# Kernel tuning notes

Measured on AMD Instinct MI355X. Metric: run time of the kernel, lower is better.

The kernel has to match this reference:

```python
import jax, jax.numpy as jnp
import numpy as np
from jax import lax

T_HORIZON = 5.0
OFFSET_X = 1.0  # longitudinal safety offset in VEH_VEH_distance
OFFSET_Y = 0.3  # lateral safety offset


def _rollout(state, dt, n_steps):
    """Unicycle Euler rollout with zero backup control (const vel, const yaw).
    state: [B, A, 4] = (x, y, yaw, v); dt: [B, A, 1]. Returns [B, A, T, 4]."""
    def step_fn(s, _):
        yaw = s[..., 2]
        v = s[..., 3]
        zeros = jnp.zeros_like(v)
        ds = jnp.stack([v * jnp.cos(yaw), v * jnp.sin(yaw), zeros, zeros], axis=-1)
        s_next = s + ds * dt
        return s_next, s_next
    _, traj = lax.scan(step_fn, state, None, length=n_steps)  # [T, B, A, 4]
    return jnp.moveaxis(traj, 0, 2)  # [B, A, T, 4]


def _veh_veh_distance(ego, agent, ego_extent, agent_extent):
    """Signed rectangle distance: agent box corners measured in ego box frame.
    ego/agent: [..., 3] = (x, y, yaw); extents: [..., 3] = (L, W, H).
    Returns per-corner signed distance [..., 4]."""
    # 4 corners of agent footprint in agent body frame
    sx = jnp.asarray([0.5, 0.5, -0.5, -0.5], dtype=ego.dtype)
    sy = jnp.asarray([0.5, -0.5, 0.5, -0.5], dtype=ego.dtype)
    cx = agent_extent[..., 0:1] * sx  # [..., 4]
    cy = agent_extent[..., 1:2] * sy
    ca, sa = jnp.cos(agent[..., 2:3]), jnp.sin(agent[..., 2:3])
    # corners in world frame
    wx = agent[..., 0:1] + cx * ca - cy * sa
    wy = agent[..., 1:2] + cx * sa + cy * ca
    # transform into ego body frame
    ce, se = jnp.cos(ego[..., 2:3]), jnp.sin(ego[..., 2:3])
    rx = wx - ego[..., 0:1]
    ry = wy - ego[..., 1:2]
    ex = rx * ce + ry * se
    ey = -rx * se + ry * ce
    dx = jnp.abs(ex) - 0.5 * ego_extent[..., 0:1] - OFFSET_X
    dy = jnp.abs(ey) - 0.5 * ego_extent[..., 1:2] - OFFSET_Y
    return jnp.maximum(dx, dy)  # [..., 4] per-corner signed box distance


def _cbf_forward(data, n_t):
    ego_state = data[..., 0:4]
    agent_state = data[..., 4:8]
    ego_extent = data[..., 8:11]
    agent_extent = data[..., 11:14]
    dt = data[..., 14:15]  # [B, A, 1]

    ego_traj = _rollout(ego_state, dt, n_t)      # [B, A, T, 4]
    agent_traj = _rollout(agent_state, dt, n_t)  # [B, A, T, 4]

    ee = ego_extent[..., None, :]    # broadcast over T
    ae = agent_extent[..., None, :]
    d_corner = _veh_veh_distance(ego_traj[..., 0:3], agent_traj[..., 0:3], ee, ae)  # [B,A,T,4]
    dist = d_corner.min(axis=-1)  # min over corners -> [B, A, T]
    h = dist.min(axis=-1)         # min over horizon  -> [B, A]
    # saturate_cbf=True
    h = (jax.nn.sigmoid(h / 5.0) - 0.5) * 10.0
    return h


def setup_inputs() -> dict:
    key = jax.random.key(0)
    ks = jax.random.split(key, 8)
    B, A = 4096, 32
    DT = 0.1

    def make_state(k0, k1, k2):
        pos = jax.random.uniform(k0, (B, A, 2), minval=-50.0, maxval=50.0)
        yaw = jax.random.uniform(k1, (B, A, 1), minval=-np.pi, maxval=np.pi)
        v = jax.random.uniform(k2, (B, A, 1), minval=0.0, maxval=15.0)
        return jnp.concatenate([pos, yaw, v], axis=-1)

    ego_state = make_state(ks[0], ks[1], ks[2])
    agent_state = make_state(ks[3], ks[4], ks[5])
    base_extent = jnp.asarray([4.5, 2.0, 1.6], dtype=jnp.float32)
    ego_extent = jnp.broadcast_to(base_extent, (B, A, 3)) * (1.0 + 0.1 * jax.random.uniform(ks[6], (B, A, 3)))
    agent_extent = jnp.broadcast_to(base_extent, (B, A, 3)) * (1.0 + 0.1 * jax.random.uniform(ks[7], (B, A, 3)))
    dt = jnp.full((B, A, 1), DT, dtype=jnp.float32)

    data = jnp.concatenate([ego_state, agent_state, ego_extent, agent_extent, dt], axis=-1)  # [B, A, 15]
    return {"data": data}


def reference(data) -> jnp.ndarray:
    n_t = int(round(T_HORIZON / float(data[0, 0, 14])))  # N_tForward = T_horizon / dt
    return _cbf_forward(data, n_t)
```

## Files before the change

### kernel.cpp

```cpp
#include <hip/hip_runtime.h>
#include <math.h>
#include <float.h>

#define OFFSET_X 1.0f
#define OFFSET_Y 0.3f
#define T_HORIZON 5.0f

__global__ __launch_bounds__(256) void BackupBarrierCBF_kernel(
    const float* __restrict__ data, float* __restrict__ out, int n)
{
    int i = blockIdx.x * blockDim.x + threadIdx.x;
    if (i >= n) return;

    const float* p = data + (size_t)i * 15;
    float ex0  = p[0],  ey0 = p[1],  eyaw = p[2],  ev = p[3];
    float ax0  = p[4],  ay0 = p[5],  ayaw = p[6],  av = p[7];
    float eL   = p[8],  eW  = p[9];
    float aL   = p[11], aW  = p[12];
    float dt   = p[14];

    int n_t = (int)roundf(T_HORIZON / dt);

    float ce, se, ca, sa;
    sincosf(eyaw, &se, &ce);
    sincosf(ayaw, &sa, &ca);

    float dvx = av * ca - ev * ce;
    float dvy = av * sa - ev * se;
    float dX  = ( dvx * ce + dvy * se) * dt;
    float dY  = (-dvx * se + dvy * ce) * dt;

    float rx0 = ax0 - ex0;
    float ry0 = ay0 - ey0;

    float hx = 0.5f * eL + OFFSET_X;
    float hy = 0.5f * eW + OFFSET_Y;
    float hcx = 0.5f * aL;
    float hcy = 0.5f * aW;

    float X[4], Y[4];
#pragma unroll
    for (int k = 0; k < 4; ++k) {
        float cx = (k < 2)        ?  hcx : -hcx;
        float cy = ((k & 1) == 0) ?  hcy : -hcy;
        float wx = rx0 + cx * ca - cy * sa;
        float wy = ry0 + cx * sa + cy * ca;
        X[k] =  wx * ce + wy * se;
        Y[k] = -wx * se + wy * ce;
    }

    float m = FLT_MAX;
    for (int t = 0; t < n_t; ++t) {
#pragma unroll
        for (int k = 0; k < 4; ++k) {
            X[k] += dX;
            Y[k] += dY;
            float d = fmaxf(fabsf(X[k]) - hx, fabsf(Y[k]) - hy);
            m = fminf(m, d);
        }
    }

    float s = 1.0f / (1.0f + expf(-m * 0.2f));
    out[i] = (s - 0.5f) * 10.0f;
}

extern "C" void kernel_launch(void* const* d_in, const int* in_sizes, int n_in,
                              void* d_out, int out_size, void* d_ws, size_t ws_size,
                              hipStream_t stream) {
    const float* data = (const float*)d_in[0];
    float* out = (float*)d_out;
    int n = out_size;
    int block = 256;
    int grid = (n + block - 1) / block;
    BackupBarrierCBF_kernel<<<grid, block, 0, stream>>>(data, out, n);
}
```

Measured before the change: 59.68 us.

## Replace time-step loop with analytic breakpoint candidates and stage inputs via LDS

```diff
diff --git a/kernel.cpp b/kernel.cpp
--- a/kernel.cpp
+++ b/kernel.cpp
@@ -9,58 +9,92 @@
 __global__ __launch_bounds__(256) void BackupBarrierCBF_kernel(
     const float* __restrict__ data, float* __restrict__ out, int n)
 {
-    int i = blockIdx.x * blockDim.x + threadIdx.x;
+    __shared__ float sdata[256 * 15];
+
+    const int tid  = threadIdx.x;
+    const int base = blockIdx.x * 256;
+    const int i    = base + tid;
+
+    const int nItems  = min(256, n - base);
+    const int nFloats = nItems * 15;
+    const float* gsrc = data + (size_t)base * 15;
+    const int nVec4   = nFloats >> 2;
+    const float4* src4 = reinterpret_cast<const float4*>(gsrc);
+    float4* dst4       = reinterpret_cast<float4*>(sdata);
+    for (int k = tid; k < nVec4; k += 256) dst4[k] = src4[k];
+    for (int k = (nVec4 << 2) + tid; k < nFloats; k += 256) sdata[k] = gsrc[k];
+    __syncthreads();
+
     if (i >= n) return;
+    const float* p = sdata + tid * 15;
 
-    const float* p = data + (size_t)i * 15;
-    float ex0  = p[0],  ey0 = p[1],  eyaw = p[2],  ev = p[3];
-    float ax0  = p[4],  ay0 = p[5],  ayaw = p[6],  av = p[7];
-    float eL   = p[8],  eW  = p[9];
-    float aL   = p[11], aW  = p[12];
-    float dt   = p[14];
+    const float ex0  = p[0],  ey0 = p[1],  eyaw = p[2],  ev = p[3];
+    const float ax0  = p[4],  ay0 = p[5],  ayaw = p[6],  av = p[7];
+    const float eL   = p[8],  eW  = p[9];
+    const float aL   = p[11], aW  = p[12];
+    const float dt   = p[14];
 
-    int n_t = (int)roundf(T_HORIZON / dt);
+    const float nf = roundf(T_HORIZON / dt);
 
     float ce, se, ca, sa;
     sincosf(eyaw, &se, &ce);
     sincosf(ayaw, &sa, &ca);
 
-    float dvx = av * ca - ev * ce;
-    float dvy = av * sa - ev * se;
-    float dX  = ( dvx * ce + dvy * se) * dt;
-    float dY  = (-dvx * se + dvy * ce) * dt;
+    const float dvx = av * ca - ev * ce;
+    const float dvy = av * sa - ev * se;
+    const float dX  = ( dvx * ce + dvy * se) * dt;
+    const float dY  = (-dvx * se + dvy * ce) * dt;
 
-    float rx0 = ax0 - ex0;
-    float ry0 = ay0 - ey0;
+    const float rx0 = ax0 - ex0;
+    const float ry0 = ay0 - ey0;
 
-    float hx = 0.5f * eL + OFFSET_X;
-    float hy = 0.5f * eW + OFFSET_Y;
-    float hcx = 0.5f * aL;
-    float hcy = 0.5f * aW;
+    const float hx  = 0.5f * eL + OFFSET_X;
+    const float hy  = 0.5f * eW + OFFSET_Y;
+    const float hcx = 0.5f * aL;
+    const float hcy = 0.5f * aW;
+    const float dh  = hx - hy;
 
-    float X[4], Y[4];
+    const float rX = __fdividef(1.0f, dX);
+    const float rY = __fdividef(1.0f, dY);
+    const float rP = __fdividef(1.0f, dX + dY);
+    const float rM = __fdividef(1.0f, dX - dY);
+
+    float m = FLT_MAX;
+
 #pragma unroll
     for (int k = 0; k < 4; ++k) {
-        float cx = (k < 2)        ?  hcx : -hcx;
-        float cy = ((k & 1) == 0) ?  hcy : -hcy;
-        float wx = rx0 + cx * ca - cy * sa;
-        float wy = ry0 + cx * sa + cy * ca;
-        X[k] =  wx * ce + wy * se;
-        Y[k] = -wx * se + wy * ce;
-    }
+        const float cx = (k < 2)        ?  hcx : -hcx;
+        const float cy = ((k & 1) == 0) ?  hcy : -hcy;
+        const float wx = rx0 + cx * ca - cy * sa;
+        const float wy = ry0 + cx * sa + cy * ca;
+        const float X0 =  wx * ce + wy * se;
+        const float Y0 = -wx * se + wy * ce;
 
-    float m = FLT_MAX;
-    for (int t = 0; t < n_t; ++t) {
+        const float S = X0 + Y0;
+        const float D = X0 - Y0;
+        const float cands[6] = {
+            -X0 * rX,
+            -Y0 * rY,
+            (dh - D) * rM,
+            (dh - S) * rP,
+            -(S + dh) * rP,
+            -(D + dh) * rM
+        };
+
 #pragma unroll
-        for (int k = 0; k < 4; ++k) {
-            X[k] += dX;
-            Y[k] += dY;
-            float d = fmaxf(fabsf(X[k]) - hx, fabsf(Y[k]) - hy);
-            m = fminf(m, d);
+        for (int c = 0; c < 6; ++c) {
+            const float tc = fminf(fmaxf(cands[c], 1.0f), nf);
+            const float t0 = floorf(tc);
+            const float t1 = fminf(t0 + 1.0f, nf);
+            const float d0 = fmaxf(fabsf(fmaf(t0, dX, X0)) - hx,
+                                   fabsf(fmaf(t0, dY, Y0)) - hy);
+            const float d1 = fmaxf(fabsf(fmaf(t1, dX, X0)) - hx,
+                                   fabsf(fmaf(t1, dY, Y0)) - hy);
+            m = fminf(m, fminf(d0, d1));
         }
     }
 
-    float s = 1.0f / (1.0f + expf(-m * 0.2f));
+    const float s = 1.0f / (1.0f + expf(-m * 0.2f));
     out[i] = (s - 0.5f) * 10.0f;
 }
 
```

Result: faster. 57.87 us (-3.0%).
